# Kernel tuning notes

Hardware: AMD Instinct MI355X
Metric: run time of the kernel (lower is better)

The kernel has to match this reference:

```python
import jax, jax.numpy as jnp
import numpy as np

EPS = 1e-5
NEG_SLOPE = 0.01  # F.leaky_relu default

N0, N1, N2 = 100000, 25000, 5000
E0, E1 = 800000, 160000
D_IN, D_HID, D_OUT = 256, 256, 128


def setup_inputs() -> dict:
    key = jax.random.key(0)
    ks = jax.random.split(key, 16)
    inp = {
        "x": jax.random.normal(ks[0], (N0, D_IN), dtype=jnp.float32),
        "src0": jax.random.randint(ks[1], (E0,), 0, N0, dtype=jnp.int32),
        "dst0": jax.random.randint(ks[2], (E0,), 0, N1, dtype=jnp.int32),
        "val0": jnp.arange(E0, dtype=jnp.int32),
        "src1": jax.random.randint(ks[3], (E1,), 0, N1, dtype=jnp.int32),
        "dst1": jax.random.randint(ks[4], (E1,), 0, N2, dtype=jnp.int32),
        "val1": jnp.arange(E1, dtype=jnp.int32),
        "timestamps": jax.random.randint(ks[5], (E0 + E1,), 0, 100, dtype=jnp.int32),
        "time": 50,
        "interval": 10,
        # SAGEConv layer 1 (in -> hidden): lin_l (bias) on aggregated, lin_r (no bias) on root
        "W1l": jax.random.normal(ks[6], (D_IN, D_HID), dtype=jnp.float32) / np.sqrt(D_IN),
        "W1r": jax.random.normal(ks[7], (D_IN, D_HID), dtype=jnp.float32) / np.sqrt(D_IN),
        "b1": jnp.zeros((D_HID,), dtype=jnp.float32),
        # BatchNorm1d params (eval mode: running stats)
        "g1": jnp.ones((D_HID,), dtype=jnp.float32),
        "bt1": jnp.zeros((D_HID,), dtype=jnp.float32),
        "rm1": jax.random.normal(ks[8], (D_HID,), dtype=jnp.float32) * 0.1,
        "rv1": jax.random.uniform(ks[9], (D_HID,), dtype=jnp.float32) + 0.5,
        # SAGEConv layer 2 (hidden -> out)
        "W2l": jax.random.normal(ks[10], (D_HID, D_OUT), dtype=jnp.float32) / np.sqrt(D_HID),
        "W2r": jax.random.normal(ks[11], (D_HID, D_OUT), dtype=jnp.float32) / np.sqrt(D_HID),
        "b2": jnp.zeros((D_OUT,), dtype=jnp.float32),
    }
    return inp


def _time_mask(val, timestamps, time, interval):
    # time_sparse keeps edges whose timestamp is in {time, ..., time+interval-1}
    ts = timestamps[val]
    return (ts >= time) & (ts < time + interval)


def _sage_conv(x_src, x_tgt, src, dst, mask, Wl, Wr, b, n_tgt):
    m = mask.astype(x_src.dtype)
    msg = x_src[src] * m[:, None]               # [E, D] gather + mask
    agg = jax.ops.segment_sum(msg, dst, num_segments=n_tgt)
    deg = jax.ops.segment_sum(m, dst, num_segments=n_tgt)
    agg = agg / jnp.maximum(deg, 1.0)[:, None]  # mean aggregation
    return agg @ Wl + b + x_tgt @ Wr


def reference(x, src0, dst0, val0, src1, dst1, val1, timestamps, time, interval,
              W1l, W1r, b1, g1, bt1, rm1, rv1, W2l, W2r, b2):
    # layer 0: N0 -> N1
    mask0 = _time_mask(val0, timestamps, time, interval)
    h = _sage_conv(x, x[:N1], src0, dst0, mask0, W1l, W1r, b1, N1)
    # BatchNorm1d (eval) + leaky_relu; dropout is identity in eval
    h = (h - rm1) * jax.lax.rsqrt(rv1 + EPS) * g1 + bt1
    h = jnp.where(h >= 0, h, NEG_SLOPE * h)
    # layer 1: N1 -> N2
    mask1 = _time_mask(val1, timestamps, time, interval)
    out = _sage_conv(h, h[:N2], src1, dst1, mask1, W2l, W2r, b2, N2)
    return out, mask1
```

## Files before the change

kernel.cpp:

```cpp
#include <hip/hip_runtime.h>

#define N1c 25000
#define N2c 5000
#define Dc 256
#define DOUTc 128
#define EPSc 1e-5f
#define NEGc 0.01f
#define CAPc 32

typedef __attribute__((ext_vector_type(8))) short short8;
typedef __attribute__((ext_vector_type(4))) float f32x4;

__device__ __forceinline__ ushort f2bf(float f) {
    unsigned u = __float_as_uint(f);
    u += 0x7fffu + ((u >> 16) & 1u);
    return (ushort)(u >> 16);
}
__device__ __forceinline__ float bf2f(ushort u) {
    return __uint_as_float(((unsigned)u) << 16);
}
__device__ __forceinline__ unsigned pack2(float lo, float hi) {
    return ((unsigned)f2bf(lo)) | (((unsigned)f2bf(hi)) << 16);
}

__global__ __launch_bounds__(256) void prep_fill(
    const int* __restrict__ src0, const int* __restrict__ dst0, const int* __restrict__ val0,
    const int* __restrict__ src1, const int* __restrict__ dst1, const int* __restrict__ val1,
    const int* __restrict__ ts, const int* __restrict__ time_p, const int* __restrict__ itv_p,
    const float* __restrict__ W1l, const float* __restrict__ W1r,
    const float* __restrict__ W2l, const float* __restrict__ W2r,
    int E0, int E1,
    ushort* __restrict__ Bt1, ushort* __restrict__ Bt2,
    int* __restrict__ cnt0, int* __restrict__ cnt1,
    int* __restrict__ eidx0, int* __restrict__ eidx1,
    float* __restrict__ mask_out) {
    const int flat = blockIdx.x * blockDim.x + threadIdx.x;
    const int NT = gridDim.x * blockDim.x;
    const int t0 = *time_p, iv = *itv_p;

    for (int i = flat; i < 256 * 512; i += NT) {
        int n = i >> 9, k = i & 511;
        float v = (k < 256) ? W1l[(size_t)k * 256 + n] : W1r[(size_t)(k - 256) * 256 + n];
        Bt1[i] = f2bf(v);
    }
    for (int i = flat; i < 128 * 512; i += NT) {
        int n = i >> 9, k = i & 511;
        float v = (k < 256) ? W2l[(size_t)k * 128 + n] : W2r[(size_t)(k - 256) * 128 + n];
        Bt2[i] = f2bf(v);
    }
    for (int e = flat; e < E0; e += NT) {
        int t = ts[val0[e]];
        if (t >= t0 && t < t0 + iv) {
            int d = dst0[e];
            int pos = atomicAdd(&cnt0[d], 1);
            if (pos < CAPc) eidx0[d * CAPc + pos] = src0[e];
        }
    }
    for (int e = flat; e < E1; e += NT) {
        int t = ts[val1[e]];
        bool m = (t >= t0 && t < t0 + iv);
        mask_out[e] = m ? 1.0f : 0.0f;
        if (m) {
            int d = dst1[e];
            int pos = atomicAdd(&cnt1[d], 1);
            if (pos < CAPc) eidx1[d * CAPc + pos] = src1[e];
        }
    }
}

__global__ void gather_f32(const float* __restrict__ X,
                           const int* __restrict__ cnt,
                           const int* __restrict__ eidx,
                           const int* __restrict__ src, const int* __restrict__ dst,
                           const int* __restrict__ val, const int* __restrict__ ts,
                           const int* __restrict__ time_p, const int* __restrict__ itv_p,
                           int E,
                           ushort* __restrict__ agg, int n) {
    int wave = (blockIdx.x * blockDim.x + threadIdx.x) >> 6;
    int lane = threadIdx.x & 63;
    if (wave >= n) return;
    int c = cnt[wave];
    float4 acc = make_float4(0.f, 0.f, 0.f, 0.f);
    float4 acc2 = make_float4(0.f, 0.f, 0.f, 0.f);
    if (c <= CAPc) {
        int my = (lane < c) ? eidx[wave * CAPc + lane] : 0;
        int j = 0;
        for (; j + 1 < c; j += 2) {
            int s0 = __shfl(my, j, 64);
            int s1 = __shfl(my, j + 1, 64);
            float4 v0 = *(const float4*)(X + (size_t)s0 * Dc + lane * 4);
            float4 v1 = *(const float4*)(X + (size_t)s1 * Dc + lane * 4);
            acc.x += v0.x; acc.y += v0.y; acc.z += v0.z; acc.w += v0.w;
            acc2.x += v1.x; acc2.y += v1.y; acc2.z += v1.z; acc2.w += v1.w;
        }
        if (j < c) {
            int s0 = __shfl(my, j, 64);
            float4 v0 = *(const float4*)(X + (size_t)s0 * Dc + lane * 4);
            acc.x += v0.x; acc.y += v0.y; acc.z += v0.z; acc.w += v0.w;
        }
    } else {
        int t0 = *time_p, iv = *itv_p;
        for (int e = 0; e < E; ++e) {
            if (dst[e] != wave) continue;
            int t = ts[val[e]];
            if (t >= t0 && t < t0 + iv) {
                float4 v = *(const float4*)(X + (size_t)src[e] * Dc + lane * 4);
                acc.x += v.x; acc.y += v.y; acc.z += v.z; acc.w += v.w;
            }
        }
    }
    acc.x += acc2.x; acc.y += acc2.y; acc.z += acc2.z; acc.w += acc2.w;
    float inv = 1.0f / fmaxf((float)c, 1.0f);
    ushort4 o;
    o.x = f2bf(acc.x * inv); o.y = f2bf(acc.y * inv);
    o.z = f2bf(acc.z * inv); o.w = f2bf(acc.w * inv);
    *(ushort4*)(agg + (size_t)wave * Dc + lane * 4) = o;
}

__global__ void gather_bf16(const ushort* __restrict__ H,
                            const int* __restrict__ cnt,
                            const int* __restrict__ eidx,
                            const int* __restrict__ src, const int* __restrict__ dst,
                            const int* __restrict__ val, const int* __restrict__ ts,
                            const int* __restrict__ time_p, const int* __restrict__ itv_p,
                            int E,
                            ushort* __restrict__ agg, int n) {
    int wave = (blockIdx.x * blockDim.x + threadIdx.x) >> 6;
    int lane = threadIdx.x & 63;
    if (wave >= n) return;
    int c = cnt[wave];
    float4 acc = make_float4(0.f, 0.f, 0.f, 0.f);
    float4 acc2 = make_float4(0.f, 0.f, 0.f, 0.f);
    if (c <= CAPc) {
        int my = (lane < c) ? eidx[wave * CAPc + lane] : 0;
        int j = 0;
        for (; j + 1 < c; j += 2) {
            int s0 = __shfl(my, j, 64);
            int s1 = __shfl(my, j + 1, 64);
            ushort4 v0 = *(const ushort4*)(H + (size_t)s0 * Dc + lane * 4);
            ushort4 v1 = *(const ushort4*)(H + (size_t)s1 * Dc + lane * 4);
            acc.x += bf2f(v0.x); acc.y += bf2f(v0.y);
            acc.z += bf2f(v0.z); acc.w += bf2f(v0.w);
            acc2.x += bf2f(v1.x); acc2.y += bf2f(v1.y);
            acc2.z += bf2f(v1.z); acc2.w += bf2f(v1.w);
        }
        if (j < c) {
            int s0 = __shfl(my, j, 64);
            ushort4 v0 = *(const ushort4*)(H + (size_t)s0 * Dc + lane * 4);
            acc.x += bf2f(v0.x); acc.y += bf2f(v0.y);
            acc.z += bf2f(v0.z); acc.w += bf2f(v0.w);
        }
    } else {
        int t0 = *time_p, iv = *itv_p;
        for (int e = 0; e < E; ++e) {
            if (dst[e] != wave) continue;
            int t = ts[val[e]];
            if (t >= t0 && t < t0 + iv) {
                ushort4 v = *(const ushort4*)(H + (size_t)src[e] * Dc + lane * 4);
                acc.x += bf2f(v.x); acc.y += bf2f(v.y);
                acc.z += bf2f(v.z); acc.w += bf2f(v.w);
            }
        }
    }
    acc.x += acc2.x; acc.y += acc2.y; acc.z += acc2.z; acc.w += acc2.w;
    float inv = 1.0f / fmaxf((float)c, 1.0f);
    ushort4 o;
    o.x = f2bf(acc.x * inv); o.y = f2bf(acc.y * inv);
    o.z = f2bf(acc.z * inv); o.w = f2bf(acc.w * inv);
    *(ushort4*)(agg + (size_t)wave * Dc + lane * 4) = o;
}

template <int VARIANT, int GRPS>
__global__ __launch_bounds__(128) void gemm_mfma(
    const ushort* __restrict__ Alo,
    const ushort* __restrict__ A2b, const float* __restrict__ A2f,
    const ushort* __restrict__ Bt,
    const float* __restrict__ bias,
    const float* __restrict__ g, const float* __restrict__ bt,
    const float* __restrict__ rm, const float* __restrict__ rv,
    void* __restrict__ Cout, int M) {
    constexpr int BM = 32 * GRPS;
    constexpr int TPR = 128 / BM;
    constexpr int CHUNK = 32 / TPR;
    __shared__ ushort As[BM][40];
    __shared__ ushort Bs[128][40];
    int tid = threadIdx.x;
    int wave = tid >> 6, lane = tid & 63;
    int quad = lane >> 4, l16 = lane & 15;
    int m0 = blockIdx.y * BM, n0 = blockIdx.x * 128;
    f32x4 acc[GRPS][8] = {};
    int ar = tid / TPR;
    int ak = (tid % TPR) * CHUNK;
    int bn = tid;
    for (int k0 = 0; k0 < 512; k0 += 32) {
        uint4 a0 = make_uint4(0, 0, 0, 0), a1 = make_uint4(0, 0, 0, 0);
        bool inb = (m0 + ar) < M;
        if (k0 < 256) {
            if (inb) {
                const ushort* Ag = Alo + (size_t)(m0 + ar) * Dc + k0 + ak;
                a0 = *(const uint4*)Ag;
                if (CHUNK == 16) a1 = *(const uint4*)(Ag + 8);
            }
        } else if (VARIANT == 0) {
            if (inb) {
                const float* Af = A2f + (size_t)(m0 + ar) * Dc + (k0 - 256) + ak;
                float4 f0 = *(const float4*)(Af + 0);
                float4 f1 = *(const float4*)(Af + 4);
                a0 = make_uint4(pack2(f0.x, f0.y), pack2(f0.z, f0.w),
                                pack2(f1.x, f1.y), pack2(f1.z, f1.w));
                if (CHUNK == 16) {
                    float4 f2 = *(const float4*)(Af + 8);
                    float4 f3 = *(const float4*)(Af + 12);
                    a1 = make_uint4(pack2(f2.x, f2.y), pack2(f2.z, f2.w),
                                    pack2(f3.x, f3.y), pack2(f3.z, f3.w));
                }
            }
        } else {
            if (inb) {
                const ushort* Ag = A2b + (size_t)(m0 + ar) * Dc + (k0 - 256) + ak;
                a0 = *(const uint4*)Ag;
                if (CHUNK == 16) a1 = *(const uint4*)(Ag + 8);
            }
        }
        const ushort* Bg = Bt + (size_t)(n0 + bn) * 512 + k0;
        uint4 b0 = *(const uint4*)(Bg + 0);
        uint4 b1 = *(const uint4*)(Bg + 8);
        uint4 b2 = *(const uint4*)(Bg + 16);
        uint4 b3 = *(const uint4*)(Bg + 24);
        __syncthreads();
        *(uint4*)&As[ar][ak] = a0;
        if (CHUNK == 16) *(uint4*)&As[ar][ak + 8] = a1;
        *(uint4*)&Bs[bn][0] = b0;
        *(uint4*)&Bs[bn][8] = b1;
        *(uint4*)&Bs[bn][16] = b2;
        *(uint4*)&Bs[bn][24] = b3;
        __syncthreads();
        short8 af[GRPS];
#pragma unroll
        for (int grp = 0; grp < GRPS; ++grp)
            af[grp] = *(const short8*)&As[wave * 16 * GRPS + grp * 16 + l16][quad * 8];
#pragma unroll
        for (int j = 0; j < 8; ++j) {
            short8 bf = *(const short8*)&Bs[j * 16 + l16][quad * 8];
#pragma unroll
            for (int grp = 0; grp < GRPS; ++grp)
                acc[grp][j] = __builtin_amdgcn_mfma_f32_16x16x32_bf16(af[grp], bf, acc[grp][j], 0, 0, 0);
        }
    }
#pragma unroll
    for (int grp = 0; grp < GRPS; ++grp) {
#pragma unroll
        for (int j = 0; j < 8; ++j) {
            int gn = n0 + j * 16 + l16;
            float sc = 1.f, sh = bias[gn];
            if (VARIANT == 0) {
                float s = g[gn] * rsqrtf(rv[gn] + EPSc);
                sh = (bias[gn] - rm[gn]) * s + bt[gn];
                sc = s;
            }
            int gmb = m0 + wave * 16 * GRPS + grp * 16 + quad * 4;
#pragma unroll
            for (int r = 0; r < 4; ++r) {
                int gm = gmb + r;
                if (gm >= M) continue;
                float v = acc[grp][j][r];
                if (VARIANT == 0) {
                    v = v * sc + sh;
                    v = v >= 0.f ? v : NEGc * v;
                    ((ushort*)Cout)[(size_t)gm * Dc + gn] = f2bf(v);
                } else {
                    ((float*)Cout)[(size_t)gm * DOUTc + gn] = v + sh;
                }
            }
        }
    }
}

extern "C" void kernel_launch(void* const* d_in, const int* in_sizes, int n_in,
                              void* d_out, int out_size, void* d_ws, size_t ws_size,
                              hipStream_t stream) {
    const float* x    = (const float*)d_in[0];
    const int* src0   = (const int*)d_in[1];
    const int* dst0   = (const int*)d_in[2];
    const int* val0   = (const int*)d_in[3];
    const int* src1   = (const int*)d_in[4];
    const int* dst1   = (const int*)d_in[5];
    const int* val1   = (const int*)d_in[6];
    const int* ts     = (const int*)d_in[7];
    const int* time_p = (const int*)d_in[8];
    const int* itv_p  = (const int*)d_in[9];
    const float* W1l  = (const float*)d_in[10];
    const float* W1r  = (const float*)d_in[11];
    const float* b1   = (const float*)d_in[12];
    const float* g1   = (const float*)d_in[13];
    const float* bt1  = (const float*)d_in[14];
    const float* rm1  = (const float*)d_in[15];
    const float* rv1  = (const float*)d_in[16];
    const float* W2l  = (const float*)d_in[17];
    const float* W2r  = (const float*)d_in[18];
    const float* b2   = (const float*)d_in[19];
    int E0 = in_sizes[1];
    int E1 = in_sizes[4];
    float* out = (float*)d_out;

    ushort* agg0 = (ushort*)d_ws;
    ushort* h    = agg0 + (size_t)N1c * Dc;
    ushort* agg1 = h    + (size_t)N1c * Dc;
    ushort* Bt1  = agg1 + (size_t)N2c * Dc;
    ushort* Bt2  = Bt1  + 256 * 512;
    int* ip      = (int*)(Bt2 + 128 * 512);
    int* cnt0    = ip;             ip += N1c;
    int* cnt1    = ip;             ip += N2c;
    int* eidx0   = ip;             ip += N1c * CAPc;
    int* eidx1   = ip;             ip += N2c * CAPc;
    float* mask_tail = out + (size_t)N2c * DOUTc;

    hipMemsetAsync(cnt0, 0, (size_t)(N1c + N2c) * sizeof(int), stream);

    prep_fill<<<2048, 256, 0, stream>>>(
        src0, dst0, val0, src1, dst1, val1, ts, time_p, itv_p,
        W1l, W1r, W2l, W2r, E0, E1, Bt1, Bt2,
        cnt0, cnt1, eidx0, eidx1, mask_tail);
    gather_f32<<<(N1c + 3) / 4, 256, 0, stream>>>(
        x, cnt0, eidx0, src0, dst0, val0, ts, time_p, itv_p, E0, agg0, N1c);
    gemm_mfma<0, 2><<<dim3(2, (N1c + 63) / 64), 128, 0, stream>>>(
        agg0, nullptr, x, Bt1, b1, g1, bt1, rm1, rv1, h, N1c);
    gather_bf16<<<(N2c + 3) / 4, 256, 0, stream>>>(
        h, cnt1, eidx1, src1, dst1, val1, ts, time_p, itv_p, E1, agg1, N2c);
    gemm_mfma<1, 1><<<dim3(1, (N2c + 31) / 32), 128, 0, stream>>>(
        agg1, h, nullptr, Bt2, b2, nullptr, nullptr, nullptr, nullptr, out, N2c);
}
```

Before: 254.2 us.

## Fuse neighbor gather-mean into MFMA GEMM via shared-memory A tile

```diff
diff --git a/kernel.cpp b/kernel.cpp
--- a/kernel.cpp
+++ b/kernel.cpp
@@ -18,9 +18,6 @@
 }
 __device__ __forceinline__ float bf2f(ushort u) {
     return __uint_as_float(((unsigned)u) << 16);
-}
-__device__ __forceinline__ unsigned pack2(float lo, float hi) {
-    return ((unsigned)f2bf(lo)) | (((unsigned)f2bf(hi)) << 16);
 }
 
 __global__ __launch_bounds__(256) void prep_fill(
@@ -68,209 +65,134 @@
     }
 }
 
-__global__ void gather_f32(const float* __restrict__ X,
-                           const int* __restrict__ cnt,
-                           const int* __restrict__ eidx,
-                           const int* __restrict__ src, const int* __restrict__ dst,
-                           const int* __restrict__ val, const int* __restrict__ ts,
-                           const int* __restrict__ time_p, const int* __restrict__ itv_p,
-                           int E,
-                           ushort* __restrict__ agg, int n) {
-    int wave = (blockIdx.x * blockDim.x + threadIdx.x) >> 6;
-    int lane = threadIdx.x & 63;
-    if (wave >= n) return;
-    int c = cnt[wave];
-    float4 acc = make_float4(0.f, 0.f, 0.f, 0.f);
-    float4 acc2 = make_float4(0.f, 0.f, 0.f, 0.f);
-    if (c <= CAPc) {
-        int my = (lane < c) ? eidx[wave * CAPc + lane] : 0;
-        int j = 0;
-        for (; j + 1 < c; j += 2) {
-            int s0 = __shfl(my, j, 64);
-            int s1 = __shfl(my, j + 1, 64);
-            float4 v0 = *(const float4*)(X + (size_t)s0 * Dc + lane * 4);
-            float4 v1 = *(const float4*)(X + (size_t)s1 * Dc + lane * 4);
-            acc.x += v0.x; acc.y += v0.y; acc.z += v0.z; acc.w += v0.w;
-            acc2.x += v1.x; acc2.y += v1.y; acc2.z += v1.z; acc2.w += v1.w;
-        }
-        if (j < c) {
-            int s0 = __shfl(my, j, 64);
-            float4 v0 = *(const float4*)(X + (size_t)s0 * Dc + lane * 4);
-            acc.x += v0.x; acc.y += v0.y; acc.z += v0.z; acc.w += v0.w;
-        }
-    } else {
-        int t0 = *time_p, iv = *itv_p;
-        for (int e = 0; e < E; ++e) {
-            if (dst[e] != wave) continue;
-            int t = ts[val[e]];
-            if (t >= t0 && t < t0 + iv) {
-                float4 v = *(const float4*)(X + (size_t)src[e] * Dc + lane * 4);
-                acc.x += v.x; acc.y += v.y; acc.z += v.z; acc.w += v.w;
-            }
-        }
-    }
-    acc.x += acc2.x; acc.y += acc2.y; acc.z += acc2.z; acc.w += acc2.w;
-    float inv = 1.0f / fmaxf((float)c, 1.0f);
-    ushort4 o;
-    o.x = f2bf(acc.x * inv); o.y = f2bf(acc.y * inv);
-    o.z = f2bf(acc.z * inv); o.w = f2bf(acc.w * inv);
-    *(ushort4*)(agg + (size_t)wave * Dc + lane * 4) = o;
-}
-
-__global__ void gather_bf16(const ushort* __restrict__ H,
-                            const int* __restrict__ cnt,
-                            const int* __restrict__ eidx,
-                            const int* __restrict__ src, const int* __restrict__ dst,
-                            const int* __restrict__ val, const int* __restrict__ ts,
-                            const int* __restrict__ time_p, const int* __restrict__ itv_p,
-                            int E,
-                            ushort* __restrict__ agg, int n) {
-    int wave = (blockIdx.x * blockDim.x + threadIdx.x) >> 6;
-    int lane = threadIdx.x & 63;
-    if (wave >= n) return;
-    int c = cnt[wave];
-    float4 acc = make_float4(0.f, 0.f, 0.f, 0.f);
-    float4 acc2 = make_float4(0.f, 0.f, 0.f, 0.f);
-    if (c <= CAPc) {
-        int my = (lane < c) ? eidx[wave * CAPc + lane] : 0;
-        int j = 0;
-        for (; j + 1 < c; j += 2) {
-            int s0 = __shfl(my, j, 64);
-            int s1 = __shfl(my, j + 1, 64);
-            ushort4 v0 = *(const ushort4*)(H + (size_t)s0 * Dc + lane * 4);
-            ushort4 v1 = *(const ushort4*)(H + (size_t)s1 * Dc + lane * 4);
-            acc.x += bf2f(v0.x); acc.y += bf2f(v0.y);
-            acc.z += bf2f(v0.z); acc.w += bf2f(v0.w);
-            acc2.x += bf2f(v1.x); acc2.y += bf2f(v1.y);
-            acc2.z += bf2f(v1.z); acc2.w += bf2f(v1.w);
-        }
-        if (j < c) {
-            int s0 = __shfl(my, j, 64);
-            ushort4 v0 = *(const ushort4*)(H + (size_t)s0 * Dc + lane * 4);
-            acc.x += bf2f(v0.x); acc.y += bf2f(v0.y);
-            acc.z += bf2f(v0.z); acc.w += bf2f(v0.w);
-        }
-    } else {
-        int t0 = *time_p, iv = *itv_p;
-        for (int e = 0; e < E; ++e) {
-            if (dst[e] != wave) continue;
-            int t = ts[val[e]];
-            if (t >= t0 && t < t0 + iv) {
-                ushort4 v = *(const ushort4*)(H + (size_t)src[e] * Dc + lane * 4);
-                acc.x += bf2f(v.x); acc.y += bf2f(v.y);
-                acc.z += bf2f(v.z); acc.w += bf2f(v.w);
-            }
-        }
-    }
-    acc.x += acc2.x; acc.y += acc2.y; acc.z += acc2.z; acc.w += acc2.w;
-    float inv = 1.0f / fmaxf((float)c, 1.0f);
-    ushort4 o;
-    o.x = f2bf(acc.x * inv); o.y = f2bf(acc.y * inv);
-    o.z = f2bf(acc.z * inv); o.w = f2bf(acc.w * inv);
-    *(ushort4*)(agg + (size_t)wave * Dc + lane * 4) = o;
-}
-
-template <int VARIANT, int GRPS>
-__global__ __launch_bounds__(128) void gemm_mfma(
-    const ushort* __restrict__ Alo,
-    const ushort* __restrict__ A2b, const float* __restrict__ A2f,
+template <int VARIANT, int NJ>
+__global__ __launch_bounds__(128) void fused_gemm(
+    const void* __restrict__ Asrc,
+    const int* __restrict__ cnt, const int* __restrict__ eidx,
+    const int* __restrict__ src, const int* __restrict__ dst,
+    const int* __restrict__ val, const int* __restrict__ ts,
+    const int* __restrict__ time_p, const int* __restrict__ itv_p, int E,
     const ushort* __restrict__ Bt,
     const float* __restrict__ bias,
     const float* __restrict__ g, const float* __restrict__ bt,
     const float* __restrict__ rm, const float* __restrict__ rv,
     void* __restrict__ Cout, int M) {
-    constexpr int BM = 32 * GRPS;
-    constexpr int TPR = 128 / BM;
-    constexpr int CHUNK = 32 / TPR;
-    __shared__ ushort As[BM][40];
-    __shared__ ushort Bs[128][40];
-    int tid = threadIdx.x;
-    int wave = tid >> 6, lane = tid & 63;
-    int quad = lane >> 4, l16 = lane & 15;
-    int m0 = blockIdx.y * BM, n0 = blockIdx.x * 128;
-    f32x4 acc[GRPS][8] = {};
-    int ar = tid / TPR;
-    int ak = (tid % TPR) * CHUNK;
-    int bn = tid;
+    __shared__ ushort As[32][536];
+    const int tid = threadIdx.x;
+    const int wave = tid >> 6, lane = tid & 63;
+    const int quad = lane >> 4, l16 = lane & 15;
+    const int m0 = blockIdx.x * 32;
+    const float* Xf = (const float*)Asrc;
+    const ushort* Hb = (const ushort*)Asrc;
+
+    for (int r8 = 0; r8 < 16; ++r8) {
+        int r = wave * 16 + r8;
+        int m = m0 + r;
+        if (m >= M) {
+            *(ushort4*)&As[r][lane * 4] = make_ushort4(0, 0, 0, 0);
+            *(ushort4*)&As[r][256 + lane * 4] = make_ushort4(0, 0, 0, 0);
+            continue;
+        }
+        int c = cnt[m];
+        int my = (lane < CAPc) ? eidx[m * CAPc + lane] : 0;
+        float4 a0 = make_float4(0.f, 0.f, 0.f, 0.f);
+        float4 a1 = make_float4(0.f, 0.f, 0.f, 0.f);
+        if (c <= CAPc) {
+            int j = 0;
+            for (; j + 1 < c; j += 2) {
+                int s0 = __shfl(my, j, 64);
+                int s1 = __shfl(my, j + 1, 64);
+                if (VARIANT == 0) {
+                    float4 v0 = *(const float4*)(Xf + (size_t)s0 * Dc + lane * 4);
+                    float4 v1 = *(const float4*)(Xf + (size_t)s1 * Dc + lane * 4);
+                    a0.x += v0.x; a0.y += v0.y; a0.z += v0.z; a0.w += v0.w;
+                    a1.x += v1.x; a1.y += v1.y; a1.z += v1.z; a1.w += v1.w;
+                } else {
+                    ushort4 v0 = *(const ushort4*)(Hb + (size_t)s0 * Dc + lane * 4);
+                    ushort4 v1 = *(const ushort4*)(Hb + (size_t)s1 * Dc + lane * 4);
+                    a0.x += bf2f(v0.x); a0.y += bf2f(v0.y); a0.z += bf2f(v0.z); a0.w += bf2f(v0.w);
+                    a1.x += bf2f(v1.x); a1.y += bf2f(v1.y); a1.z += bf2f(v1.z); a1.w += bf2f(v1.w);
+                }
+            }
+            if (j < c) {
+                int s0 = __shfl(my, j, 64);
+                if (VARIANT == 0) {
+                    float4 v0 = *(const float4*)(Xf + (size_t)s0 * Dc + lane * 4);
+                    a0.x += v0.x; a0.y += v0.y; a0.z += v0.z; a0.w += v0.w;
+                } else {
+                    ushort4 v0 = *(const ushort4*)(Hb + (size_t)s0 * Dc + lane * 4);
+                    a0.x += bf2f(v0.x); a0.y += bf2f(v0.y); a0.z += bf2f(v0.z); a0.w += bf2f(v0.w);
+                }
+            }
+        } else {
+            int t0 = *time_p, iv = *itv_p;
+            for (int e = 0; e < E; ++e) {
+                if (dst[e] != m) continue;
+                int t = ts[val[e]];
+                if (t >= t0 && t < t0 + iv) {
+                    if (VARIANT == 0) {
+                        float4 v = *(const float4*)(Xf + (size_t)src[e] * Dc + lane * 4);
+                        a0.x += v.x; a0.y += v.y; a0.z += v.z; a0.w += v.w;
+                    } else {
+                        ushort4 v = *(const ushort4*)(Hb + (size_t)src[e] * Dc + lane * 4);
+                        a0.x += bf2f(v.x); a0.y += bf2f(v.y); a0.z += bf2f(v.z); a0.w += bf2f(v.w);
+                    }
+                }
+            }
+        }
+        a0.x += a1.x; a0.y += a1.y; a0.z += a1.z; a0.w += a1.w;
+        float inv = 1.0f / fmaxf((float)c, 1.0f);
+        ushort4 o;
+        o.x = f2bf(a0.x * inv); o.y = f2bf(a0.y * inv);
+        o.z = f2bf(a0.z * inv); o.w = f2bf(a0.w * inv);
+        *(ushort4*)&As[r][lane * 4] = o;
+        if (VARIANT == 0) {
+            float4 rt = *(const float4*)(Xf + (size_t)m * Dc + lane * 4);
+            ushort4 ro;
+            ro.x = f2bf(rt.x); ro.y = f2bf(rt.y); ro.z = f2bf(rt.z); ro.w = f2bf(rt.w);
+            *(ushort4*)&As[r][256 + lane * 4] = ro;
+        } else {
+            *(ushort4*)&As[r][256 + lane * 4] = *(const ushort4*)(Hb + (size_t)m * Dc + lane * 4);
+        }
+    }
+    __syncthreads();
+
+    f32x4 acc[NJ] = {};
+    const ushort* Bw = Bt + (size_t)l16 * 512 + quad * 8;
     for (int k0 = 0; k0 < 512; k0 += 32) {
-        uint4 a0 = make_uint4(0, 0, 0, 0), a1 = make_uint4(0, 0, 0, 0);
-        bool inb = (m0 + ar) < M;
-        if (k0 < 256) {
-            if (inb) {
-                const ushort* Ag = Alo + (size_t)(m0 + ar) * Dc + k0 + ak;
-                a0 = *(const uint4*)Ag;
-                if (CHUNK == 16) a1 = *(const uint4*)(Ag + 8);
-            }
-        } else if (VARIANT == 0) {
-            if (inb) {
-                const float* Af = A2f + (size_t)(m0 + ar) * Dc + (k0 - 256) + ak;
-                float4 f0 = *(const float4*)(Af + 0);
-                float4 f1 = *(const float4*)(Af + 4);
-                a0 = make_uint4(pack2(f0.x, f0.y), pack2(f0.z, f0.w),
-                                pack2(f1.x, f1.y), pack2(f1.z, f1.w));
-                if (CHUNK == 16) {
-                    float4 f2 = *(const float4*)(Af + 8);
-                    float4 f3 = *(const float4*)(Af + 12);
-                    a1 = make_uint4(pack2(f2.x, f2.y), pack2(f2.z, f2.w),
-                                    pack2(f3.x, f3.y), pack2(f3.z, f3.w));
-                }
-            }
-        } else {
-            if (inb) {
-                const ushort* Ag = A2b + (size_t)(m0 + ar) * Dc + (k0 - 256) + ak;
-                a0 = *(const uint4*)Ag;
-                if (CHUNK == 16) a1 = *(const uint4*)(Ag + 8);
-            }
-        }
-        const ushort* Bg = Bt + (size_t)(n0 + bn) * 512 + k0;
-        uint4 b0 = *(const uint4*)(Bg + 0);
-        uint4 b1 = *(const uint4*)(Bg + 8);
-        uint4 b2 = *(const uint4*)(Bg + 16);
-        uint4 b3 = *(const uint4*)(Bg + 24);
-        __syncthreads();
-        *(uint4*)&As[ar][ak] = a0;
-        if (CHUNK == 16) *(uint4*)&As[ar][ak + 8] = a1;
-        *(uint4*)&Bs[bn][0] = b0;
-        *(uint4*)&Bs[bn][8] = b1;
-        *(uint4*)&Bs[bn][16] = b2;
-        *(uint4*)&Bs[bn][24] = b3;
-        __syncthreads();
-        short8 af[GRPS];
-#pragma unroll
-        for (int grp = 0; grp < GRPS; ++grp)
-            af[grp] = *(const short8*)&As[wave * 16 * GRPS + grp * 16 + l16][quad * 8];
-#pragma unroll
-        for (int j = 0; j < 8; ++j) {
-            short8 bf = *(const short8*)&Bs[j * 16 + l16][quad * 8];
-#pragma unroll
-            for (int grp = 0; grp < GRPS; ++grp)
-                acc[grp][j] = __builtin_amdgcn_mfma_f32_16x16x32_bf16(af[grp], bf, acc[grp][j], 0, 0, 0);
-        }
-    }
-#pragma unroll
-    for (int grp = 0; grp < GRPS; ++grp) {
-#pragma unroll
-        for (int j = 0; j < 8; ++j) {
-            int gn = n0 + j * 16 + l16;
-            float sc = 1.f, sh = bias[gn];
+        short8 af = *(const short8*)&As[wave * 16 + l16][k0 + quad * 8];
+        uint4 bfr[NJ];
+#pragma unroll
+        for (int j = 0; j < NJ; ++j)
+            bfr[j] = *(const uint4*)(Bw + (size_t)j * 16 * 512 + k0);
+#pragma unroll
+        for (int j = 0; j < NJ; ++j) {
+            short8 bf = *reinterpret_cast<const short8*>(&bfr[j]);
+            acc[j] = __builtin_amdgcn_mfma_f32_16x16x32_bf16(af, bf, acc[j], 0, 0, 0);
+        }
+    }
+
+#pragma unroll
+    for (int j = 0; j < NJ; ++j) {
+        int gn = j * 16 + l16;
+        float sc = 1.f, sh = bias[gn];
+        if (VARIANT == 0) {
+            float s = g[gn] * rsqrtf(rv[gn] + EPSc);
+            sh = (bias[gn] - rm[gn]) * s + bt[gn];
+            sc = s;
+        }
+        int gmb = m0 + wave * 16 + quad * 4;
+#pragma unroll
+        for (int rr = 0; rr < 4; ++rr) {
+            int gm = gmb + rr;
+            if (gm >= M) continue;
+            float v = acc[j][rr];
             if (VARIANT == 0) {
-                float s = g[gn] * rsqrtf(rv[gn] + EPSc);
-                sh = (bias[gn] - rm[gn]) * s + bt[gn];
-                sc = s;
-            }
-            int gmb = m0 + wave * 16 * GRPS + grp * 16 + quad * 4;
-#pragma unroll
-            for (int r = 0; r < 4; ++r) {
-                int gm = gmb + r;
-                if (gm >= M) continue;
-                float v = acc[grp][j][r];
-                if (VARIANT == 0) {
-                    v = v * sc + sh;
-                    v = v >= 0.f ? v : NEGc * v;
-                    ((ushort*)Cout)[(size_t)gm * Dc + gn] = f2bf(v);
-                } else {
-                    ((float*)Cout)[(size_t)gm * DOUTc + gn] = v + sh;
-                }
+                v = v * sc + sh;
+                v = v >= 0.f ? v : NEGc * v;
+                ((ushort*)Cout)[(size_t)gm * Dc + gn] = f2bf(v);
+            } else {
+                ((float*)Cout)[(size_t)gm * DOUTc + gn] = v + sh;
             }
         }
     }
@@ -303,10 +225,8 @@
     int E1 = in_sizes[4];
     float* out = (float*)d_out;
 
-    ushort* agg0 = (ushort*)d_ws;
-    ushort* h    = agg0 + (size_t)N1c * Dc;
-    ushort* agg1 = h    + (size_t)N1c * Dc;
-    ushort* Bt1  = agg1 + (size_t)N2c * Dc;
+    ushort* h    = (ushort*)d_ws;
+    ushort* Bt1  = h    + (size_t)N1c * Dc;
     ushort* Bt2  = Bt1  + 256 * 512;
     int* ip      = (int*)(Bt2 + 128 * 512);
     int* cnt0    = ip;             ip += N1c;
@@ -321,12 +241,10 @@
         src0, dst0, val0, src1, dst1, val1, ts, time_p, itv_p,
         W1l, W1r, W2l, W2r, E0, E1, Bt1, Bt2,
         cnt0, cnt1, eidx0, eidx1, mask_tail);
-    gather_f32<<<(N1c + 3) / 4, 256, 0, stream>>>(
-        x, cnt0, eidx0, src0, dst0, val0, ts, time_p, itv_p, E0, agg0, N1c);
-    gemm_mfma<0, 2><<<dim3(2, (N1c + 63) / 64), 128, 0, stream>>>(
-        agg0, nullptr, x, Bt1, b1, g1, bt1, rm1, rv1, h, N1c);
-    gather_bf16<<<(N2c + 3) / 4, 256, 0, stream>>>(
-        h, cnt1, eidx1, src1, dst1, val1, ts, time_p, itv_p, E1, agg1, N2c);
-    gemm_mfma<1, 1><<<dim3(1, (N2c + 31) / 32), 128, 0, stream>>>(
-        agg1, h, nullptr, Bt2, b2, nullptr, nullptr, nullptr, nullptr, out, N2c);
-}
+    fused_gemm<0, 16><<<(N1c + 31) / 32, 128, 0, stream>>>(
+        x, cnt0, eidx0, src0, dst0, val0, ts, time_p, itv_p, E0,
+        Bt1, b1, g1, bt1, rm1, rv1, h, N1c);
+    fused_gemm<1, 8><<<(N2c + 31) / 32, 128, 0, stream>>>(
+        h, cnt1, eidx1, src1, dst1, val1, ts, time_p, itv_p, E1,
+        Bt2, b2, nullptr, nullptr, nullptr, nullptr, out, N2c);
+}
```

New measurement: 325.6 us. 28.1% more time.
